# Kernel optimization log

Hardware: AMD Instinct MI355X
Metric: run time of the kernel (lower is better)

Reference implementation:

```python
import jax, jax.numpy as jnp
import numpy as np

NUM_NODES = 50000
NUM_EDGES = 800000
IN_CH = 128
OUT_CH = 128


def setup_inputs() -> dict:
    key = jax.random.key(0)
    k1, k2, k3 = jax.random.split(key, 3)
    x = jax.random.normal(k1, (NUM_NODES, IN_CH), dtype=jnp.float32)
    # xavier_uniform-like init for weight
    limit = float(np.sqrt(6.0 / (IN_CH + OUT_CH)))
    weight = jax.random.uniform(k2, (IN_CH, OUT_CH), dtype=jnp.float32, minval=-limit, maxval=limit)
    edge_index = jax.random.randint(k3, (2, NUM_EDGES), 0, NUM_NODES, dtype=jnp.int64)
    return {"x": x, "weight": weight, "edge_index": edge_index}


def reference(x, weight, edge_index):
    # GCN-style layer: out = D^{-1/2} A D^{-1/2} x W, with A built from COO edges
    # (duplicate edges sum, matching torch sparse_coo_tensor coalescing).
    num_nodes = x.shape[0]
    row, col = edge_index[0], edge_index[1]
    ones = jnp.ones(edge_index.shape[1], dtype=x.dtype)
    deg = jax.ops.segment_sum(ones, row, num_segments=num_nodes)  # row-sum of A
    deg = jnp.where(deg == 0, jnp.asarray(1.0, x.dtype), deg)
    dinv = deg ** -0.5  # [N]
    coef = dinv[row] * dinv[col]  # per-edge normalized value [E]
    msgs = x[col] * coef[:, None]  # gather + scale, [E, C_in]
    agg = jax.ops.segment_sum(msgs, row, num_segments=num_nodes)  # scatter-add, [N, C_in]
    return agg @ weight  # [N, C_out]
```

## Files before the change

### kernel.cpp

```cpp
#include <hip/hip_runtime.h>

#define N_NODES 50000
#define N_EDGES 800000
#define CH 128
#define SLOT 64
#define FB ((N_EDGES + 255) / 256)
#define GB ((N_NODES + 63) / 64)
#define GRID (GB * 5)

typedef __attribute__((ext_vector_type(8))) short bf16x8;
typedef __attribute__((ext_vector_type(4))) float f32x4;

static __device__ inline unsigned f2bf(float f) {
    union { float f; unsigned u; } v; v.f = f;
    unsigned r = v.u + 0x7fff + ((v.u >> 16) & 1);
    return r >> 16;
}
static __device__ inline float bflo(unsigned v) { union { unsigned u; float f; } c; c.u = v << 16; return c.f; }
static __device__ inline float bfhi(unsigned v) { union { unsigned u; float f; } c; c.u = v & 0xffff0000u; return c.f; }

__global__ __launch_bounds__(256) void k_fg(const int* __restrict__ rowv,
                                            const int* __restrict__ colv,
                                            const float* __restrict__ x,
                                            const float* __restrict__ W,
                                            int* __restrict__ cursor,
                                            unsigned short* __restrict__ csrP,
                                            unsigned short* __restrict__ yh) {
    int gidx = blockIdx.x;
    bool is_gemm = (gidx % 5) == 2;

    if (!is_gemm) {
        int fill_id = gidx - (gidx + 2) / 5;
        int e = fill_id * 256 + threadIdx.x;
        if (e < N_EDGES) {
            int r = rowv[e], c = colv[e];
            int pos = atomicAdd(&cursor[r], 1);
            if (pos < SLOT) csrP[r * SLOT + pos] = (unsigned short)c;
        }
        return;
    }

    int row0 = (gidx / 5) * 64;
    int t = threadIdx.x;
    int lane = t & 63, w = t >> 6;
    int m = lane & 15, q = lane >> 4;

    int row = row0 + 16 * w + m;
    int rc = row < N_NODES ? row : N_NODES - 1;
    const float4* xr = (const float4*)(x + (size_t)rc * CH);
    bf16x8 afr[4];
    #pragma unroll
    for (int kk = 0; kk < 4; ++kk) {
        float4 a0 = xr[kk * 8 + q * 2];
        float4 a1 = xr[kk * 8 + q * 2 + 1];
        bf16x8 a;
        a[0] = (short)f2bf(a0.x); a[1] = (short)f2bf(a0.y);
        a[2] = (short)f2bf(a0.z); a[3] = (short)f2bf(a0.w);
        a[4] = (short)f2bf(a1.x); a[5] = (short)f2bf(a1.y);
        a[6] = (short)f2bf(a1.z); a[7] = (short)f2bf(a1.w);
        afr[kk] = a;
    }

    f32x4 acc[8];
    #pragma unroll
    for (int c = 0; c < 8; ++c) acc[c] = (f32x4){0.f, 0.f, 0.f, 0.f};

    #pragma unroll
    for (int c = 0; c < 8; ++c) {
        int n = c * 16 + m;
        #pragma unroll
        for (int kk = 0; kk < 4; ++kk) {
            int k0 = kk * 32 + q * 8;
            bf16x8 b;
            #pragma unroll
            for (int j = 0; j < 8; ++j)
                b[j] = (short)f2bf(W[(size_t)(k0 + j) * CH + n]);
            acc[c] = __builtin_amdgcn_mfma_f32_16x16x32_bf16(afr[kk], b, acc[c], 0, 0, 0);
        }
    }

    #pragma unroll
    for (int c = 0; c < 8; ++c) {
        #pragma unroll
        for (int r = 0; r < 4; ++r) {
            int orow = row0 + 16 * w + q * 4 + r;
            if (orow < N_NODES)
                yh[(size_t)orow * CH + c * 16 + m] = (unsigned short)f2bf(acc[c][r]);
        }
    }
}

__global__ __launch_bounds__(256) void k_agg(const int* __restrict__ cursor,
                                             const unsigned short* __restrict__ csrP,
                                             const unsigned short* __restrict__ yh,
                                             float* __restrict__ out) {
    int gid = blockIdx.x * 256 + threadIdx.x;
    int n = gid >> 6;
    int lane = threadIdx.x & 63;
    if (n >= N_NODES) return;
    int deg = cursor[n];
    int cnt = deg < SLOT ? deg : SLOT;
    float dr = rsqrtf((float)(deg > 0 ? deg : 1));
    const unsigned* __restrict__ y2 = (const unsigned*)yh;
    const uint4* __restrict__ crow = (const uint4*)(csrP + (size_t)n * SLOT);
    float ax = 0.f, ay = 0.f;
    int j = 0;
    for (; j + 8 <= cnt; j += 8) {
        uint4 cc = crow[j >> 3];
        int c0 = cc.x & 0xffff, c1 = cc.x >> 16;
        int c2 = cc.y & 0xffff, c3 = cc.y >> 16;
        int c4 = cc.z & 0xffff, c5 = cc.z >> 16;
        int c6 = cc.w & 0xffff, c7 = cc.w >> 16;
        int d0 = cursor[c0], d1 = cursor[c1], d2 = cursor[c2], d3 = cursor[c3];
        int d4 = cursor[c4], d5 = cursor[c5], d6 = cursor[c6], d7 = cursor[c7];
        float w0 = rsqrtf((float)(d0 > 0 ? d0 : 1));
        float w1 = rsqrtf((float)(d1 > 0 ? d1 : 1));
        float w2 = rsqrtf((float)(d2 > 0 ? d2 : 1));
        float w3 = rsqrtf((float)(d3 > 0 ? d3 : 1));
        float w4 = rsqrtf((float)(d4 > 0 ? d4 : 1));
        float w5 = rsqrtf((float)(d5 > 0 ? d5 : 1));
        float w6 = rsqrtf((float)(d6 > 0 ? d6 : 1));
        float w7 = rsqrtf((float)(d7 > 0 ? d7 : 1));
        unsigned v0 = y2[c0 * 64 + lane];
        unsigned v1 = y2[c1 * 64 + lane];
        unsigned v2 = y2[c2 * 64 + lane];
        unsigned v3 = y2[c3 * 64 + lane];
        unsigned v4 = y2[c4 * 64 + lane];
        unsigned v5 = y2[c5 * 64 + lane];
        unsigned v6 = y2[c6 * 64 + lane];
        unsigned v7 = y2[c7 * 64 + lane];
        ax = fmaf(bflo(v0), w0, ax); ay = fmaf(bfhi(v0), w0, ay);
        ax = fmaf(bflo(v1), w1, ax); ay = fmaf(bfhi(v1), w1, ay);
        ax = fmaf(bflo(v2), w2, ax); ay = fmaf(bfhi(v2), w2, ay);
        ax = fmaf(bflo(v3), w3, ax); ay = fmaf(bfhi(v3), w3, ay);
        ax = fmaf(bflo(v4), w4, ax); ay = fmaf(bfhi(v4), w4, ay);
        ax = fmaf(bflo(v5), w5, ax); ay = fmaf(bfhi(v5), w5, ay);
        ax = fmaf(bflo(v6), w6, ax); ay = fmaf(bfhi(v6), w6, ay);
        ax = fmaf(bflo(v7), w7, ax); ay = fmaf(bfhi(v7), w7, ay);
    }
    for (; j < cnt; ++j) {
        int c = csrP[(size_t)n * SLOT + j];
        int d = cursor[c];
        float wc = rsqrtf((float)(d > 0 ? d : 1));
        unsigned v = y2[c * 64 + lane];
        ax = fmaf(bflo(v), wc, ax); ay = fmaf(bfhi(v), wc, ay);
    }
    ((float2*)out)[n * 64 + lane] = make_float2(ax * dr, ay * dr);
}

extern "C" void kernel_launch(void* const* d_in, const int* in_sizes, int n_in,
                              void* d_out, int out_size, void* d_ws, size_t ws_size,
                              hipStream_t stream) {
    const float* x = (const float*)d_in[0];
    const float* W = (const float*)d_in[1];
    const int* edge = (const int*)d_in[2];
    const int* rowv = edge;
    const int* colv = edge + N_EDGES;
    float* out = (float*)d_out;

    char* p = (char*)d_ws;
    int* cursor = (int*)p;                         p += (size_t)N_NODES * 4;
    p = (char*)(((uintptr_t)p + 255) & ~(uintptr_t)255);
    unsigned short* csrP = (unsigned short*)p;     p += (size_t)N_NODES * SLOT * 2;
    unsigned short* yh   = (unsigned short*)p;

    hipMemsetAsync(cursor, 0, (size_t)N_NODES * sizeof(int), stream);

    k_fg <<<GRID, 256, 0, stream>>>(rowv, colv, x, W, cursor, csrP, yh);
    k_agg<<<(N_NODES * 64 + 255) / 256, 256, 0, stream>>>(cursor, csrP, yh, out);
}
```

Before: 160.1 us.

## Pad degree counters, pre-transpose weights to bf16, and batch two edges per thread

Adds a prep kernel that zeroes the cursor array, replacing the memset, and writes a transposed bf16 copy of W. The GEMM blocks can then load B fragments as vectors instead of converting strided fp32 loads for every block. Degree counters are padded to a 64-byte stride so atomics on different nodes do not share a cache line. Each fill thread now handles two edges, which changes the fill/GEMM block ratio from 4:1 to 2:1. The padding costs extra memory traffic for zeroing and makes the degree lookups in aggregation more scattered, and the extra launch adds overhead.

```diff
diff --git a/kernel.cpp b/kernel.cpp
--- a/kernel.cpp
+++ b/kernel.cpp
@@ -4,9 +4,9 @@
 #define N_EDGES 800000
 #define CH 128
 #define SLOT 64
-#define FB ((N_EDGES + 255) / 256)
+#define CSTRIDE 16
 #define GB ((N_NODES + 63) / 64)
-#define GRID (GB * 5)
+#define GRID (GB * 3)
 
 typedef __attribute__((ext_vector_type(8))) short bf16x8;
 typedef __attribute__((ext_vector_type(4))) float f32x4;
@@ -19,28 +19,46 @@
 static __device__ inline float bflo(unsigned v) { union { unsigned u; float f; } c; c.u = v << 16; return c.f; }
 static __device__ inline float bfhi(unsigned v) { union { unsigned u; float f; } c; c.u = v & 0xffff0000u; return c.f; }
 
+__global__ __launch_bounds__(256) void k_prep(const float* __restrict__ W,
+                                              unsigned short* __restrict__ wT,
+                                              int* __restrict__ cursor) {
+    int t = blockIdx.x * 256 + threadIdx.x;
+    int4 z = {0, 0, 0, 0};
+    for (int i = t; i < N_NODES * CSTRIDE / 4; i += (int)gridDim.x * 256)
+        ((int4*)cursor)[i] = z;
+    if (t < CH * CH) {
+        int n = t >> 7, k = t & 127;
+        wT[t] = (unsigned short)f2bf(W[k * CH + n]);
+    }
+}
+
 __global__ __launch_bounds__(256) void k_fg(const int* __restrict__ rowv,
                                             const int* __restrict__ colv,
                                             const float* __restrict__ x,
-                                            const float* __restrict__ W,
+                                            const unsigned short* __restrict__ wT,
                                             int* __restrict__ cursor,
                                             unsigned short* __restrict__ csrP,
                                             unsigned short* __restrict__ yh) {
     int gidx = blockIdx.x;
-    bool is_gemm = (gidx % 5) == 2;
+    bool is_gemm = (gidx % 3) == 2;
 
     if (!is_gemm) {
-        int fill_id = gidx - (gidx + 2) / 5;
-        int e = fill_id * 256 + threadIdx.x;
-        if (e < N_EDGES) {
-            int r = rowv[e], c = colv[e];
-            int pos = atomicAdd(&cursor[r], 1);
-            if (pos < SLOT) csrP[r * SLOT + pos] = (unsigned short)c;
-        }
+        int fill_id = gidx - gidx / 3;
+        int e0 = fill_id * 512 + threadIdx.x;
+        int e1 = e0 + 256;
+        bool v0 = e0 < N_EDGES, v1 = e1 < N_EDGES;
+        int r0 = 0, c0 = 0, r1 = 0, c1 = 0;
+        if (v0) { r0 = rowv[e0]; c0 = colv[e0]; }
+        if (v1) { r1 = rowv[e1]; c1 = colv[e1]; }
+        int pos0 = SLOT, pos1 = SLOT;
+        if (v0) pos0 = atomicAdd(&cursor[r0 * CSTRIDE], 1);
+        if (v1) pos1 = atomicAdd(&cursor[r1 * CSTRIDE], 1);
+        if (v0 && pos0 < SLOT) csrP[r0 * SLOT + pos0] = (unsigned short)c0;
+        if (v1 && pos1 < SLOT) csrP[r1 * SLOT + pos1] = (unsigned short)c1;
         return;
     }
 
-    int row0 = (gidx / 5) * 64;
+    int row0 = (gidx / 3) * 64;
     int t = threadIdx.x;
     int lane = t & 63, w = t >> 6;
     int m = lane & 15, q = lane >> 4;
@@ -68,15 +86,10 @@
     #pragma unroll
     for (int c = 0; c < 8; ++c) {
         int n = c * 16 + m;
+        const bf16x8* wrow = (const bf16x8*)(wT + (size_t)n * CH);
         #pragma unroll
-        for (int kk = 0; kk < 4; ++kk) {
-            int k0 = kk * 32 + q * 8;
-            bf16x8 b;
-            #pragma unroll
-            for (int j = 0; j < 8; ++j)
-                b[j] = (short)f2bf(W[(size_t)(k0 + j) * CH + n]);
-            acc[c] = __builtin_amdgcn_mfma_f32_16x16x32_bf16(afr[kk], b, acc[c], 0, 0, 0);
-        }
+        for (int kk = 0; kk < 4; ++kk)
+            acc[c] = __builtin_amdgcn_mfma_f32_16x16x32_bf16(afr[kk], wrow[kk * 4 + q], acc[c], 0, 0, 0);
     }
 
     #pragma unroll
@@ -98,7 +111,7 @@
     int n = gid >> 6;
     int lane = threadIdx.x & 63;
     if (n >= N_NODES) return;
-    int deg = cursor[n];
+    int deg = cursor[n * CSTRIDE];
     int cnt = deg < SLOT ? deg : SLOT;
     float dr = rsqrtf((float)(deg > 0 ? deg : 1));
     const unsigned* __restrict__ y2 = (const unsigned*)yh;
@@ -111,8 +124,10 @@
         int c2 = cc.y & 0xffff, c3 = cc.y >> 16;
         int c4 = cc.z & 0xffff, c5 = cc.z >> 16;
         int c6 = cc.w & 0xffff, c7 = cc.w >> 16;
-        int d0 = cursor[c0], d1 = cursor[c1], d2 = cursor[c2], d3 = cursor[c3];
-        int d4 = cursor[c4], d5 = cursor[c5], d6 = cursor[c6], d7 = cursor[c7];
+        int d0 = cursor[c0 * CSTRIDE], d1 = cursor[c1 * CSTRIDE];
+        int d2 = cursor[c2 * CSTRIDE], d3 = cursor[c3 * CSTRIDE];
+        int d4 = cursor[c4 * CSTRIDE], d5 = cursor[c5 * CSTRIDE];
+        int d6 = cursor[c6 * CSTRIDE], d7 = cursor[c7 * CSTRIDE];
         float w0 = rsqrtf((float)(d0 > 0 ? d0 : 1));
         float w1 = rsqrtf((float)(d1 > 0 ? d1 : 1));
         float w2 = rsqrtf((float)(d2 > 0 ? d2 : 1));
@@ -140,7 +155,7 @@
     }
     for (; j < cnt; ++j) {
         int c = csrP[(size_t)n * SLOT + j];
-        int d = cursor[c];
+        int d = cursor[c * CSTRIDE];
         float wc = rsqrtf((float)(d > 0 ? d : 1));
         unsigned v = y2[c * 64 + lane];
         ax = fmaf(bflo(v), wc, ax); ay = fmaf(bfhi(v), wc, ay);
@@ -159,13 +174,13 @@
     float* out = (float*)d_out;
 
     char* p = (char*)d_ws;
-    int* cursor = (int*)p;                         p += (size_t)N_NODES * 4;
+    int* cursor = (int*)p;                         p += (size_t)N_NODES * CSTRIDE * 4;
     p = (char*)(((uintptr_t)p + 255) & ~(uintptr_t)255);
+    unsigned short* wT = (unsigned short*)p;       p += (size_t)CH * CH * 2;
     unsigned short* csrP = (unsigned short*)p;     p += (size_t)N_NODES * SLOT * 2;
     unsigned short* yh   = (unsigned short*)p;
 
-    hipMemsetAsync(cursor, 0, (size_t)N_NODES * sizeof(int), stream);
-
-    k_fg <<<GRID, 256, 0, stream>>>(rowv, colv, x, W, cursor, csrP, yh);
-    k_agg<<<(N_NODES * 64 + 255) / 256, 256, 0, stream>>>(cursor, csrP, yh, out);
+    k_prep<<<512, 256, 0, stream>>>(W, wT, cursor);
+    k_fg  <<<GRID, 256, 0, stream>>>(rowv, colv, x, wT, cursor, csrP, yh);
+    k_agg <<<(N_NODES * 64 + 255) / 256, 256, 0, stream>>>(cursor, csrP, yh, out);
 }
```

After: 164.6 us. 1.03x slower.
